# Kernel tuning notes

Measured on AMD Instinct MI355X. Metric: run time of the kernel, lower is better.

The kernel has to match this reference:

```python
import jax, jax.numpy as jnp
import numpy as np

H = 2048      # hidden_size
NH = 16       # num_attention_heads
HD = H // NH  # head_dim = 128
B, S = 2, 2048
ROPE_BASE = 10000.0


def setup_inputs() -> dict:
    key = jax.random.key(0)
    ks = jax.random.split(key, 9)
    init = 0.02
    inp = {
        "hidden_states": jax.random.normal(ks[0], (B, S, H), dtype=jnp.float32),
        # torch nn.Linear weights are [out_features, in_features]
        "wq": jax.random.normal(ks[1], (H, H), dtype=jnp.float32) * init,
        "bq": jnp.zeros((H,), dtype=jnp.float32),
        "wk": jax.random.normal(ks[2], (H, H), dtype=jnp.float32) * init,
        "bk": jnp.zeros((H,), dtype=jnp.float32),
        "wv": jax.random.normal(ks[3], (H, H), dtype=jnp.float32) * init,
        "bv": jnp.zeros((H,), dtype=jnp.float32),
        "wo": jax.random.normal(ks[4], (H, H), dtype=jnp.float32) * init,
        "bo": jnp.zeros((H,), dtype=jnp.float32),
    }
    return inp


def _rope_cos_sin(seq_len, dim, dtype):
    # standard RoPE tables: [seq_len, dim]
    inv_freq = 1.0 / (ROPE_BASE ** (jnp.arange(0, dim, 2, dtype=jnp.float32) / dim))
    freqs = jnp.arange(seq_len, dtype=jnp.float32)[:, None] * inv_freq[None, :]
    emb = jnp.concatenate([freqs, freqs], axis=-1)  # [S, dim]
    return jnp.cos(emb).astype(dtype), jnp.sin(emb).astype(dtype)


def _rotate_half(x):
    half = x.shape[-1] // 2
    return jnp.concatenate([-x[..., half:], x[..., :half]], axis=-1)


def reference(hidden_states, wq, bq, wk, bk, wv, bv, wo, bo):
    b, s, h = hidden_states.shape
    scale = HD ** -0.5

    def proj(x, w, bias):
        y = jnp.einsum("bsh,oh->bso", x, w) + bias
        # -> [b, nh, s, hd]
        return y.reshape(b, s, NH, HD).transpose(0, 2, 1, 3)

    q = proj(hidden_states, wq, bq)
    k = proj(hidden_states, wk, bk)
    v = proj(hidden_states, wv, bv)

    # rotary embeddings on q, k
    cos, sin = _rope_cos_sin(s, HD, q.dtype)  # [s, hd]
    q = q * cos + _rotate_half(q) * sin
    k = k * cos + _rotate_half(k) * sin

    # causal additive mask [s, s]
    mask = jnp.triu(jnp.full((s, s), -1e9, dtype=q.dtype), k=1)

    scores = jnp.einsum("bhqd,bhkd->bhqk", q, k) * scale + mask
    probs = jax.nn.softmax(scores, axis=-1)
    attn = jnp.einsum("bhqk,bhkd->bhqd", probs, v)
    attn = attn.transpose(0, 2, 1, 3).reshape(b, s, h)
    out = jnp.einsum("bsh,oh->bso", attn, wo) + bo
    return out
```

## Files before the change

### kernel.cpp

```cpp
#include <hip/hip_runtime.h>

typedef unsigned short u16;
typedef __attribute__((ext_vector_type(8))) __bf16 bf16x8;
typedef __attribute__((ext_vector_type(4))) float f32x4;
typedef __attribute__((ext_vector_type(4))) u16 u16x4;
typedef __attribute__((ext_vector_type(8))) u16 u16x8;

constexpr int S = 2048;
constexpr int H = 2048;
constexpr int NH = 16;
constexpr int HD = 128;
constexpr int M = 4096;
constexpr float SCALE = 0.08838834764831845f;

__device__ __forceinline__ u16 f2bf(float f) {
  union { float f; unsigned u; } v; v.f = f;
  unsigned r = v.u + 0x7fffu + ((v.u >> 16) & 1u);
  return (u16)(r >> 16);
}
__device__ __forceinline__ float bf2f(u16 u) {
  union { unsigned u; float f; } v; v.u = ((unsigned)u) << 16;
  return v.f;
}
__device__ __forceinline__ unsigned cvt_pk_bf16(float lo, float hi) {
  unsigned r;
  asm("v_cvt_pk_bf16_f32 %0, %1, %2" : "=v"(r) : "v"(lo), "v"(hi));
  return r;
}
__device__ __forceinline__ float fract_f(float x) {
  float o; asm("v_fract_f32 %0, %1" : "=v"(o) : "v"(x)); return o;
}
__device__ __forceinline__ float sin_rev(float x) {
  float o; asm("v_sin_f32 %0, %1" : "=v"(o) : "v"(x)); return o;
}
__device__ __forceinline__ float cos_rev(float x) {
  float o; asm("v_cos_f32 %0, %1" : "=v"(o) : "v"(x)); return o;
}
__device__ __forceinline__ f32x4 MFMA16(bf16x8 a, bf16x8 b, f32x4 c) {
  return __builtin_amdgcn_mfma_f32_16x16x32_bf16(a, b, c, 0, 0, 0);
}

__device__ __forceinline__ void gld16(const u16* g, u16* l) {
  __builtin_amdgcn_global_load_lds(
      (const __attribute__((address_space(1))) void*)g,
      (__attribute__((address_space(3))) void*)l, 16, 0, 0);
}

#define SBAR  { __builtin_amdgcn_sched_barrier(0); __builtin_amdgcn_s_barrier(); __builtin_amdgcn_sched_barrier(0); }
#define LGKM0 { asm volatile("s_waitcnt lgkmcnt(0)" ::: "memory"); __builtin_amdgcn_sched_barrier(0); }

__global__ __launch_bounds__(256) void prep_kernel(const float* __restrict__ x,
                                                   const float* __restrict__ wq,
                                                   const float* __restrict__ wk,
                                                   const float* __restrict__ wv,
                                                   const float* __restrict__ wo,
                                                   const float* __restrict__ bq,
                                                   const float* __restrict__ bk,
                                                   const float* __restrict__ bv,
                                                   u16* __restrict__ xb,
                                                   u16* __restrict__ wqkvb,
                                                   u16* __restrict__ wob,
                                                   float* __restrict__ bqkv) {
  const int NX = (M * H) / 1024;
  const int NW = (H * H) / 1024;
  int bid = blockIdx.x;
  if (bid < NX) {
    int i = (bid * 256 + threadIdx.x) * 4;
    float4 v = *(const float4*)(x + i);
    u16x4 o;
    o[0] = f2bf(v.x); o[1] = f2bf(v.y); o[2] = f2bf(v.z); o[3] = f2bf(v.w);
    *(u16x4*)(xb + i) = o;
    return;
  }
  bid -= NX;
  if (bid < 4 * NW) {
    const int z = bid / NW, lb = bid % NW;
    const float* in;
    u16* out;
    switch (z) {
      case 0: in = wq; out = wqkvb; break;
      case 1: in = wk; out = wqkvb + (size_t)H * H; break;
      case 2: in = wv; out = wqkvb + 2ull * H * H; break;
      default: in = wo; out = wob; break;
    }
    int i = (lb * 256 + threadIdx.x) * 4;
    int ro = i >> 11, cb = i & 2047;
    int rin = ro;
    if (z < 2) {
      int nd = ro & 127;
      int od = (nd & 1) ? (nd >> 1) + 64 : (nd >> 1);
      rin = (ro & ~127) | od;
    }
    float4 v = *(const float4*)(in + (size_t)rin * H + cb);
    u16x4 o;
    o[0] = f2bf(v.x); o[1] = f2bf(v.y); o[2] = f2bf(v.z); o[3] = f2bf(v.w);
    *(u16x4*)(out + i) = o;
    return;
  }
  bid -= 4 * NW;
  int i = bid * 256 + threadIdx.x;
  if (i < 4096) {
    const float* src = (i < 2048) ? bq : bk;
    int base = i & 2047;
    int nd = base & 127;
    int od = (nd & 1) ? (nd >> 1) + 64 : (nd >> 1);
    bqkv[i] = src[(base & ~127) | od];
  } else {
    bqkv[i] = bv[i & 2047];
  }
}

template<int NW, int EMODE>
__device__ __forceinline__ void gemm_body(const u16* __restrict__ A,
                                          const u16* __restrict__ Bw,
                                          const float* __restrict__ bias,
                                          void* __restrict__ out0, void* __restrict__ out1,
                                          void* __restrict__ out2,
                                          int brow, int bcol,
                                          u16* AsL, u16* BsL) {
  const int t = threadIdx.x;
  const int w = t >> 6, l = t & 63;
  const int wr = w >> 2, wc = w & 3;
  const int lr = l & 15, lg = l >> 4;
  const int swz = lr & 7;

  f32x4 acc[8][NW] = {};
  bf16x8 af[4], b0[NW], b1[NW];

  const int sr = t >> 3, sj = t & 7;

  auto STAGE_A = [&](int BUF, int HALF, int TILE) {
    u16* d = AsL + BUF * (256 * 64) + HALF * (128 * 64);
    const u16* sp = A + (size_t)(brow + HALF * 128) * H + TILE * 64;
    gld16(sp + (size_t)sr * H        + ((sj ^ (sr & 7)) * 8), d + t * 8);
    gld16(sp + (size_t)(64 + sr) * H + ((sj ^ (sr & 7)) * 8), d + (512 + t) * 8);
  };
  auto STAGE_B = [&](int BUF, int TILE) {
    u16* d = BsL + BUF * (NW * 64 * 64);
    const u16* sp = Bw + (size_t)bcol * H + TILE * 64;
    #pragma unroll
    for (int i = 0; i < NW; ++i)
      gld16(sp + (size_t)(i * 64 + sr) * H + ((sj ^ (sr & 7)) * 8),
            d + (i * 512 + t) * 8);
  };
  auto LDA = [&](int BUF, int KH, int MB) {
    const u16* base = AsL + BUF * (256 * 64) + (wr * 128 + MB * 16 + lr) * 64;
    #pragma unroll
    for (int i = 0; i < 4; ++i)
      af[i] = *(const bf16x8*)(base + i * (16 * 64) + (((KH * 4 + lg) ^ swz) * 8));
  };
  auto LDB = [&](int BUF, int KH, bf16x8* bb) {
    const u16* base = BsL + BUF * (NW * 64 * 64) + (wc * (NW * 16) + lr) * 64;
    #pragma unroll
    for (int n = 0; n < NW; ++n)
      bb[n] = *(const bf16x8*)(base + n * (16 * 64) + (((KH * 4 + lg) ^ swz) * 8));
  };
  auto MM = [&](int MB, bf16x8* bb) {
    __builtin_amdgcn_s_setprio(1);
    #pragma unroll
    for (int i = 0; i < 4; ++i)
      #pragma unroll
      for (int n = 0; n < NW; ++n)
        acc[MB + i][n] = MFMA16(af[i], bb[n], acc[MB + i][n]);
    __builtin_amdgcn_s_setprio(0);
  };
  auto GATE = [&]() {
    if constexpr (NW == 3) { asm volatile("s_waitcnt vmcnt(3)" ::: "memory"); }
    else                   { asm volatile("s_waitcnt vmcnt(2)" ::: "memory"); }
  };

  STAGE_A(0, 0, 0); STAGE_A(0, 1, 0);
  STAGE_B(0, 0);
  STAGE_B(1, 1);
  GATE();
  SBAR;

  for (int J = 0; J < 16; ++J) {
    const int u = 2 * J;
    const bool more = (J < 15);
    LDA(0, 0, 0); LDB(0, 0, b0);
    STAGE_A(1, 0, u + 1);
    SBAR; LGKM0; MM(0, b0); SBAR;
    LDA(0, 0, 4);
    STAGE_A(1, 1, u + 1);
    SBAR; LGKM0; MM(4, b0); SBAR;
    LDA(0, 1, 0); LDB(0, 1, b1);
    SBAR; LGKM0; MM(0, b1); SBAR;
    LDA(0, 1, 4);
    if (more) STAGE_B(0, u + 2);
    SBAR; LGKM0; MM(4, b1);
    if (more) { GATE(); } else { asm volatile("s_waitcnt vmcnt(0)" ::: "memory"); }
    SBAR;
    LDA(1, 0, 0); LDB(1, 0, b0);
    if (more) STAGE_A(0, 0, u + 2);
    SBAR; LGKM0; MM(0, b0); SBAR;
    LDA(1, 0, 4);
    if (more) STAGE_A(0, 1, u + 2);
    SBAR; LGKM0; MM(4, b0); SBAR;
    LDA(1, 1, 0); LDB(1, 1, b1);
    SBAR; LGKM0; MM(0, b1); SBAR;
    LDA(1, 1, 4);
    if (more) STAGE_B(1, u + 3);
    SBAR; LGKM0; MM(4, b1);
    if (more) { GATE(); SBAR; }
  }

  float frv[NW];
  if constexpr (EMODE == 3) {
    #pragma unroll
    for (int n = 0; n < NW; ++n) {
      const int col = ((bcol & 2047) + wc * (NW * 16) + n * 16 + lr);
      const int d = (col & 127) >> 1;
      frv[n] = __builtin_amdgcn_exp2f(-(float)d * 0.20762050593f) * 0.15915494309f;
    }
  }
  #pragma unroll
  for (int m = 0; m < 8; ++m) {
    const int row0 = brow + wr * 128 + m * 16 + lg * 4;
    #pragma unroll
    for (int n = 0; n < NW; ++n) {
      const int gcol0 = bcol + wc * (NW * 16) + n * 16;
      const float bv2 = bias[gcol0 + lr];
      if constexpr (EMODE == 0) {
        float* C = (float*)out0;
        #pragma unroll
        for (int r = 0; r < 4; ++r)
          C[(size_t)(row0 + r) * H + gcol0 + lr] = acc[m][n][r] + bv2;
      } else {
        const int sel = gcol0 >> 11;
        const int col = (gcol0 & 2047) + lr;
        if (sel < 2) {
          u16* Cq = sel ? (u16*)out1 : (u16*)out0;
          const float scl = sel ? 1.f : SCALE;
          #pragma unroll
          for (int r = 0; r < 4; ++r) {
            const int row = row0 + r;
            const float sv = (float)(row & (S - 1));
            float xv = acc[m][n][r] + bv2;
            float pr = __shfl_xor(xv, 1);
            float ang = fract_f(sv * frv[n]);
            float cs = cos_rev(ang), sn = sin_rev(ang);
            float o = (lr & 1) ? (xv * cs + pr * sn)
                               : (xv * cs - pr * sn);
            Cq[(size_t)row * H + col] = f2bf(o * scl);
          }
        } else {
          const int hh = col >> 7, d = col & 127;
          const int b = row0 >> 11, s0 = row0 & (S - 1);
          u16x4 pk;
          #pragma unroll
          for (int r = 0; r < 4; ++r) pk[r] = f2bf(acc[m][n][r] + bv2);
          *(u16x4*)((u16*)out2 + ((size_t)((b * 16 + hh) * 128 + d)) * S + s0) = pk;
        }
      }
    }
  }
}

__global__ __launch_bounds__(512, 2) void gemm_qkv8(const u16* __restrict__ xb,
                                                    const u16* __restrict__ wqkv,
                                                    const float* __restrict__ bqkv,
                                                    u16* Qb, u16* Kb, u16* Vt) {
  __shared__ u16 AsL[2 * 256 * 64];
  __shared__ u16 BsL[2 * 192 * 64];
  const int id = blockIdx.x;
  const int xcd = id & 7, sid = id >> 3;
  const int bx = xcd * 4 + (sid & 3), by = sid >> 2;
  gemm_body<3, 3>(xb, wqkv, bqkv, Qb, Kb, Vt, by * 256, bx * 192, AsL, BsL);
}

__global__ __launch_bounds__(512, 2) void gemm_o8(const u16* __restrict__ A,
                                                  const u16* __restrict__ W,
                                                  const float* __restrict__ bias,
                                                  float* __restrict__ C) {
  __shared__ u16 AsL[2 * 256 * 64];
  __shared__ u16 BsL[2 * 128 * 64];
  const int id = blockIdx.x;
  const int xcd = id & 7, sid = id >> 3;
  const int bx = xcd * 2 + (sid & 1), by = sid >> 1;
  gemm_body<2, 0>(A, W, bias, C, nullptr, nullptr, by * 256, bx * 128, AsL, BsL);
}

__global__ __launch_bounds__(256) void attn_fwd(const u16* __restrict__ Q,
                                                const u16* __restrict__ Kx,
                                                const u16* __restrict__ Vt,
                                                u16* __restrict__ O) {
  const int id = blockIdx.x;
  const int xcd = id & 7, slot = id >> 3;
  const int bh = (slot >> 4) * 8 + xcd;
  const int pid = slot & 15;
  const int b = bh >> 4, h = bh & 15;
  const int t = threadIdx.x, w = t >> 6, l = t & 63;
  const int lr = l & 15, lg = l >> 4;
  const int swz = lr & 7;

  __shared__ u16 Ks[2][64 * 128];
  __shared__ u16 Vs[2][128 * 64];
  __shared__ u16 P_lds[4][16 * 64];
  u16* pw = &P_lds[w][0];

  const u16* kbase = Kx + (size_t)(b * S) * H + h * HD;
  const u16* vbase = Vt + (size_t)bh * HD * S;

  auto stageK = [&](int bf, int k0) {
    #pragma unroll
    for (int it = 0; it < 4; ++it) {
      int c = it * 256 + t;
      int row = c >> 4, j = c & 15;
      gld16(kbase + (size_t)(k0 + row) * H + ((j ^ (row & 7)) * 8), &Ks[bf][0] + c * 8);
    }
  };
  auto stageV = [&](int bf, int k0) {
    #pragma unroll
    for (int it = 0; it < 4; ++it) {
      int c = it * 256 + t;
      int row = c >> 3, j = c & 7;
      gld16(vbase + (size_t)row * S + k0 + ((j ^ (row & 7)) * 8), &Vs[bf][0] + c * 8);
    }
  };

  int cur = 0;
  for (int qi = 0; qi < 2; ++qi) {
    const int qt = qi ? pid : (31 - pid);
    const int q0 = qt * 64 + w * 16;

    bf16x8 qa[4];
    const u16* qbase = Q + (size_t)(b * S + q0 + lr) * H + h * HD;
    #pragma unroll
    for (int ks = 0; ks < 4; ++ks)
      qa[ks] = *(const bf16x8*)(qbase + ks * 32 + lg * 8);

    f32x4 acc[8] = {};
    float mrun[4], lrun[4];
    #pragma unroll
    for (int r = 0; r < 4; ++r) { mrun[r] = -1e30f; lrun[r] = 0.f; }

    __syncthreads();
    stageK(cur, 0);
    stageV(cur, 0);
    __syncthreads();

    for (int kt = 0; kt <= qt; ++kt) {
      if (kt < qt) {
        stageK(cur ^ 1, (kt + 1) * 64);
        stageV(cur ^ 1, (kt + 1) * 64);
      }
      const u16* kl = &Ks[cur][0];
      const u16* vl = &Vs[cur][0];

      f32x4 sc[4] = {};
      __builtin_amdgcn_s_setprio(1);
      #pragma unroll
      for (int ks = 0; ks < 4; ++ks) {
        #pragma unroll
        for (int f = 0; f < 4; ++f) {
          bf16x8 kf = *(const bf16x8*)(kl + (f * 16 + lr) * 128 + (((ks * 4 + lg) ^ swz) * 8));
          sc[f] = __builtin_amdgcn_mfma_f32_16x16x32_bf16(qa[ks], kf, sc[f], 0, 0, 0);
        }
      }
      __builtin_amdgcn_s_setprio(0);
      const bool diag = (kt == qt);
      float p[4][4];
      #pragma unroll
      for (int f = 0; f < 4; ++f)
        #pragma unroll
        for (int r = 0; r < 4; ++r) {
          float v = sc[f][r];
          if (diag && (f * 16 + lr > w * 16 + lg * 4 + r)) v = -1e30f;
          p[f][r] = v;
        }
      float mx[4];
      #pragma unroll
      for (int r = 0; r < 4; ++r) {
        float m0 = fmaxf(fmaxf(p[0][r], p[1][r]), fmaxf(p[2][r], p[3][r]));
        m0 = fmaxf(m0, __shfl_xor(m0, 1));
        m0 = fmaxf(m0, __shfl_xor(m0, 2));
        m0 = fmaxf(m0, __shfl_xor(m0, 4));
        m0 = fmaxf(m0, __shfl_xor(m0, 8));
        mx[r] = m0;
      }
      bool grow = (mx[0] > mrun[0] + 8.f) || (mx[1] > mrun[1] + 8.f) ||
                  (mx[2] > mrun[2] + 8.f) || (mx[3] > mrun[3] + 8.f);
      if (__any(grow)) {
        float resc[4];
        #pragma unroll
        for (int r = 0; r < 4; ++r) {
          float mnew = fmaxf(mrun[r], mx[r]);
          resc[r] = __expf(mrun[r] - mnew);
          mrun[r] = mnew;
          lrun[r] *= resc[r];
        }
        #pragma unroll
        for (int fd = 0; fd < 8; ++fd) {
          f32x4 a = acc[fd];
          a[0] *= resc[0]; a[1] *= resc[1]; a[2] *= resc[2]; a[3] *= resc[3];
          acc[fd] = a;
        }
      }
      #pragma unroll
      for (int r = 0; r < 4; ++r) {
        float sum = 0.f;
        #pragma unroll
        for (int f = 0; f < 4; ++f) {
          float e = __expf(p[f][r] - mrun[r]);
          p[f][r] = e;
          sum += e;
        }
        sum += __shfl_xor(sum, 1);
        sum += __shfl_xor(sum, 2);
        sum += __shfl_xor(sum, 4);
        sum += __shfl_xor(sum, 8);
        lrun[r] += sum;
      }
      {
        const int r0 = lg * 4;
        #pragma unroll
        for (int f = 0; f < 4; ++f) {
          const int col = f * 16 + lr;
          unsigned w01 = cvt_pk_bf16(p[f][0], p[f][1]);
          unsigned w23 = cvt_pk_bf16(p[f][2], p[f][3]);
          pw[(r0 + 0) * 64 + (col ^ (((r0 + 0) & 7) << 3))] = (u16)(w01 & 0xffffu);
          pw[(r0 + 1) * 64 + (col ^ (((r0 + 1) & 7) << 3))] = (u16)(w01 >> 16);
          pw[(r0 + 2) * 64 + (col ^ (((r0 + 2) & 7) << 3))] = (u16)(w23 & 0xffffu);
          pw[(r0 + 3) * 64 + (col ^ (((r0 + 3) & 7) << 3))] = (u16)(w23 >> 16);
        }
      }
      __builtin_amdgcn_s_setprio(1);
      #pragma unroll
      for (int ks = 0; ks < 2; ++ks) {
        int col0 = ks * 32 + lg * 8;
        bf16x8 pa = *(const bf16x8*)(pw + lr * 64 + (col0 ^ (swz << 3)));
        #pragma unroll
        for (int fd = 0; fd < 8; ++fd) {
          bf16x8 vb = *(const bf16x8*)(vl + (fd * 16 + lr) * 64 + (((ks * 4 + lg) ^ swz) * 8));
          acc[fd] = __builtin_amdgcn_mfma_f32_16x16x32_bf16(pa, vb, acc[fd], 0, 0, 0);
        }
      }
      __builtin_amdgcn_s_setprio(0);
      __syncthreads();
      cur ^= 1;
    }

    u16* ob = O + (size_t)(b * S + q0 + lg * 4) * H + h * HD;
    #pragma unroll
    for (int r = 0; r < 4; ++r) {
      float inv = 1.f / lrun[r];
      #pragma unroll
      for (int fd = 0; fd < 8; ++fd)
        ob[(size_t)r * H + fd * 16 + lr] = f2bf(acc[fd][r] * inv);
    }
  }
}

extern "C" void kernel_launch(void* const* d_in, const int* in_sizes, int n_in,
                              void* d_out, int out_size, void* d_ws, size_t ws_size,
                              hipStream_t stream) {
  const float* x  = (const float*)d_in[0];
  const float* wq = (const float*)d_in[1];
  const float* bq = (const float*)d_in[2];
  const float* wk = (const float*)d_in[3];
  const float* bk = (const float*)d_in[4];
  const float* wv = (const float*)d_in[5];
  const float* bv = (const float*)d_in[6];
  const float* wo = (const float*)d_in[7];
  const float* bo = (const float*)d_in[8];

  char* ws = (char*)d_ws;
  u16*   xb    = (u16*)(ws);
  u16*   wqkvb = (u16*)(ws + (16ull << 20));
  u16*   wob   = (u16*)(ws + (40ull << 20));
  u16*   Qb    = (u16*)(ws + (48ull << 20));
  u16*   Kb    = (u16*)(ws + (64ull << 20));
  u16*   Vt    = (u16*)(ws + (80ull << 20));
  u16*   Ob    = (u16*)(ws + (96ull << 20));
  float* bqkv  = (float*)(ws + (112ull << 20));

  const int NPREP = (M * H) / 1024 + 4 * (H * H) / 1024 + 24;
  prep_kernel<<<NPREP, 256, 0, stream>>>(x, wq, wk, wv, wo, bq, bk, bv,
                                         xb, wqkvb, wob, bqkv);

  gemm_qkv8<<<512, 512, 0, stream>>>(xb, wqkvb, bqkv, Qb, Kb, Vt);

  attn_fwd<<<512, 256, 0, stream>>>(Qb, Kb, Vt, Ob);

  gemm_o8<<<256, 512, 0, stream>>>(Ob, wob, bo, (float*)d_out);
}
```

Measured before the change: 263.9 us.

## Enlarge attention query tile to 128 rows with 32 rows per warp

Each attention block now handles one 128-row query tile, with each warp owning two 16-row MFMA subtiles. Every staged K/V tile therefore feeds twice as many queries, which halves K/V global and LDS traffic per query. The earlier scheme, where one block ran two paired 64-row tiles back to back for load balance, is replaced by one tile per block, scheduled longest-first. This trades more registers per thread (launch bounds set to 2 blocks) and less even per-block work for better data reuse.

```diff
diff --git a/kernel.cpp b/kernel.cpp
--- a/kernel.cpp
+++ b/kernel.cpp
@@ -281,14 +281,15 @@
   gemm_body<2, 0>(A, W, bias, C, nullptr, nullptr, by * 256, bx * 128, AsL, BsL);
 }
 
-__global__ __launch_bounds__(256) void attn_fwd(const u16* __restrict__ Q,
-                                                const u16* __restrict__ Kx,
-                                                const u16* __restrict__ Vt,
-                                                u16* __restrict__ O) {
+__global__ __launch_bounds__(256, 2) void attn_fwd(const u16* __restrict__ Q,
+                                                   const u16* __restrict__ Kx,
+                                                   const u16* __restrict__ Vt,
+                                                   u16* __restrict__ O) {
   const int id = blockIdx.x;
-  const int xcd = id & 7, slot = id >> 3;
-  const int bh = (slot >> 4) * 8 + xcd;
-  const int pid = slot & 15;
+  const int xcd = id & 7, rest = id >> 3;
+  const int bh = (rest & 3) * 8 + xcd;
+  const int j = rest >> 2;
+  const int qt = (j < 8) ? (15 - j) : (j - 8);
   const int b = bh >> 4, h = bh & 15;
   const int t = threadIdx.x, w = t >> 6, l = t & 63;
   const int lr = l & 15, lg = l >> 4;
@@ -296,7 +297,7 @@
 
   __shared__ u16 Ks[2][64 * 128];
   __shared__ u16 Vs[2][128 * 64];
-  __shared__ u16 P_lds[4][16 * 64];
+  __shared__ u16 P_lds[4][32 * 64];
   u16* pw = &P_lds[w][0];
 
   const u16* kbase = Kx + (size_t)(b * S) * H + h * HD;
@@ -306,148 +307,183 @@
     #pragma unroll
     for (int it = 0; it < 4; ++it) {
       int c = it * 256 + t;
-      int row = c >> 4, j = c & 15;
-      gld16(kbase + (size_t)(k0 + row) * H + ((j ^ (row & 7)) * 8), &Ks[bf][0] + c * 8);
+      int row = c >> 4, jj = c & 15;
+      gld16(kbase + (size_t)(k0 + row) * H + ((jj ^ (row & 7)) * 8), &Ks[bf][0] + c * 8);
     }
   };
   auto stageV = [&](int bf, int k0) {
     #pragma unroll
     for (int it = 0; it < 4; ++it) {
       int c = it * 256 + t;
-      int row = c >> 3, j = c & 7;
-      gld16(vbase + (size_t)row * S + k0 + ((j ^ (row & 7)) * 8), &Vs[bf][0] + c * 8);
-    }
-  };
+      int row = c >> 3, jj = c & 7;
+      gld16(vbase + (size_t)row * S + k0 + ((jj ^ (row & 7)) * 8), &Vs[bf][0] + c * 8);
+    }
+  };
+
+  const int q0 = qt * 128 + w * 32;
+
+  bf16x8 qa[2][4];
+  #pragma unroll
+  for (int s2 = 0; s2 < 2; ++s2) {
+    const u16* qbase = Q + (size_t)(b * S + q0 + s2 * 16 + lr) * H + h * HD;
+    #pragma unroll
+    for (int ks = 0; ks < 4; ++ks)
+      qa[s2][ks] = *(const bf16x8*)(qbase + ks * 32 + lg * 8);
+  }
+
+  f32x4 acc0[8] = {}, acc1[8] = {};
+  float mrun[2][4], lrun[2][4];
+  #pragma unroll
+  for (int s2 = 0; s2 < 2; ++s2)
+    #pragma unroll
+    for (int r = 0; r < 4; ++r) { mrun[s2][r] = -1e30f; lrun[s2][r] = 0.f; }
 
   int cur = 0;
-  for (int qi = 0; qi < 2; ++qi) {
-    const int qt = qi ? pid : (31 - pid);
-    const int q0 = qt * 64 + w * 16;
-
-    bf16x8 qa[4];
-    const u16* qbase = Q + (size_t)(b * S + q0 + lr) * H + h * HD;
-    #pragma unroll
-    for (int ks = 0; ks < 4; ++ks)
-      qa[ks] = *(const bf16x8*)(qbase + ks * 32 + lg * 8);
-
-    f32x4 acc[8] = {};
-    float mrun[4], lrun[4];
-    #pragma unroll
-    for (int r = 0; r < 4; ++r) { mrun[r] = -1e30f; lrun[r] = 0.f; }
-
-    __syncthreads();
-    stageK(cur, 0);
-    stageV(cur, 0);
-    __syncthreads();
-
-    for (int kt = 0; kt <= qt; ++kt) {
-      if (kt < qt) {
-        stageK(cur ^ 1, (kt + 1) * 64);
-        stageV(cur ^ 1, (kt + 1) * 64);
-      }
-      const u16* kl = &Ks[cur][0];
-      const u16* vl = &Vs[cur][0];
-
-      f32x4 sc[4] = {};
-      __builtin_amdgcn_s_setprio(1);
-      #pragma unroll
-      for (int ks = 0; ks < 4; ++ks) {
-        #pragma unroll
-        for (int f = 0; f < 4; ++f) {
-          bf16x8 kf = *(const bf16x8*)(kl + (f * 16 + lr) * 128 + (((ks * 4 + lg) ^ swz) * 8));
-          sc[f] = __builtin_amdgcn_mfma_f32_16x16x32_bf16(qa[ks], kf, sc[f], 0, 0, 0);
+  const int NT = 2 * qt + 2;
+  stageK(cur, 0);
+  stageV(cur, 0);
+  __syncthreads();
+
+  for (int kt = 0; kt < NT; ++kt) {
+    if (kt < NT - 1) {
+      stageK(cur ^ 1, (kt + 1) * 64);
+      stageV(cur ^ 1, (kt + 1) * 64);
+    }
+    const u16* kl = &Ks[cur][0];
+    const u16* vl = &Vs[cur][0];
+    const int k0 = kt * 64;
+
+    f32x4 sc0[4] = {}, sc1[4] = {};
+    __builtin_amdgcn_s_setprio(1);
+    #pragma unroll
+    for (int ks = 0; ks < 4; ++ks) {
+      #pragma unroll
+      for (int f = 0; f < 4; ++f) {
+        bf16x8 kf = *(const bf16x8*)(kl + (f * 16 + lr) * 128 + (((ks * 4 + lg) ^ swz) * 8));
+        sc0[f] = MFMA16(qa[0][ks], kf, sc0[f]);
+        sc1[f] = MFMA16(qa[1][ks], kf, sc1[f]);
+      }
+    }
+    __builtin_amdgcn_s_setprio(0);
+
+    const bool maskt = (kt >= 2 * qt);
+    float p[2][4][4];
+    #pragma unroll
+    for (int f = 0; f < 4; ++f)
+      #pragma unroll
+      for (int r = 0; r < 4; ++r) {
+        float v0 = sc0[f][r], v1 = sc1[f][r];
+        if (maskt) {
+          const int col = k0 + f * 16 + lr;
+          const int row0a = q0 + lg * 4 + r;
+          if (col > row0a) v0 = -1e30f;
+          if (col > row0a + 16) v1 = -1e30f;
         }
-      }
-      __builtin_amdgcn_s_setprio(0);
-      const bool diag = (kt == qt);
-      float p[4][4];
-      #pragma unroll
-      for (int f = 0; f < 4; ++f)
-        #pragma unroll
-        for (int r = 0; r < 4; ++r) {
-          float v = sc[f][r];
-          if (diag && (f * 16 + lr > w * 16 + lg * 4 + r)) v = -1e30f;
-          p[f][r] = v;
-        }
-      float mx[4];
+        p[0][f][r] = v0;
+        p[1][f][r] = v1;
+      }
+
+    float mx[2][4];
+    #pragma unroll
+    for (int s2 = 0; s2 < 2; ++s2)
       #pragma unroll
       for (int r = 0; r < 4; ++r) {
-        float m0 = fmaxf(fmaxf(p[0][r], p[1][r]), fmaxf(p[2][r], p[3][r]));
+        float m0 = fmaxf(fmaxf(p[s2][0][r], p[s2][1][r]), fmaxf(p[s2][2][r], p[s2][3][r]));
         m0 = fmaxf(m0, __shfl_xor(m0, 1));
         m0 = fmaxf(m0, __shfl_xor(m0, 2));
         m0 = fmaxf(m0, __shfl_xor(m0, 4));
         m0 = fmaxf(m0, __shfl_xor(m0, 8));
-        mx[r] = m0;
-      }
-      bool grow = (mx[0] > mrun[0] + 8.f) || (mx[1] > mrun[1] + 8.f) ||
-                  (mx[2] > mrun[2] + 8.f) || (mx[3] > mrun[3] + 8.f);
-      if (__any(grow)) {
-        float resc[4];
+        mx[s2][r] = m0;
+      }
+    bool grow = false;
+    #pragma unroll
+    for (int s2 = 0; s2 < 2; ++s2)
+      #pragma unroll
+      for (int r = 0; r < 4; ++r)
+        grow = grow || (mx[s2][r] > mrun[s2][r] + 8.f);
+    if (__any(grow)) {
+      float resc[2][4];
+      #pragma unroll
+      for (int s2 = 0; s2 < 2; ++s2)
         #pragma unroll
         for (int r = 0; r < 4; ++r) {
-          float mnew = fmaxf(mrun[r], mx[r]);
-          resc[r] = __expf(mrun[r] - mnew);
-          mrun[r] = mnew;
-          lrun[r] *= resc[r];
+          float mnew = fmaxf(mrun[s2][r], mx[s2][r]);
+          resc[s2][r] = __expf(mrun[s2][r] - mnew);
+          mrun[s2][r] = mnew;
+          lrun[s2][r] *= resc[s2][r];
         }
-        #pragma unroll
-        for (int fd = 0; fd < 8; ++fd) {
-          f32x4 a = acc[fd];
-          a[0] *= resc[0]; a[1] *= resc[1]; a[2] *= resc[2]; a[3] *= resc[3];
-          acc[fd] = a;
-        }
-      }
+      #pragma unroll
+      for (int fd = 0; fd < 8; ++fd) {
+        f32x4 a = acc0[fd];
+        a[0] *= resc[0][0]; a[1] *= resc[0][1]; a[2] *= resc[0][2]; a[3] *= resc[0][3];
+        acc0[fd] = a;
+        f32x4 c = acc1[fd];
+        c[0] *= resc[1][0]; c[1] *= resc[1][1]; c[2] *= resc[1][2]; c[3] *= resc[1][3];
+        acc1[fd] = c;
+      }
+    }
+    #pragma unroll
+    for (int s2 = 0; s2 < 2; ++s2)
       #pragma unroll
       for (int r = 0; r < 4; ++r) {
         float sum = 0.f;
         #pragma unroll
         for (int f = 0; f < 4; ++f) {
-          float e = __expf(p[f][r] - mrun[r]);
-          p[f][r] = e;
+          float e = __expf(p[s2][f][r] - mrun[s2][r]);
+          p[s2][f][r] = e;
           sum += e;
         }
         sum += __shfl_xor(sum, 1);
         sum += __shfl_xor(sum, 2);
         sum += __shfl_xor(sum, 4);
         sum += __shfl_xor(sum, 8);
-        lrun[r] += sum;
-      }
-      {
-        const int r0 = lg * 4;
-        #pragma unroll
-        for (int f = 0; f < 4; ++f) {
-          const int col = f * 16 + lr;
-          unsigned w01 = cvt_pk_bf16(p[f][0], p[f][1]);
-          unsigned w23 = cvt_pk_bf16(p[f][2], p[f][3]);
-          pw[(r0 + 0) * 64 + (col ^ (((r0 + 0) & 7) << 3))] = (u16)(w01 & 0xffffu);
-          pw[(r0 + 1) * 64 + (col ^ (((r0 + 1) & 7) << 3))] = (u16)(w01 >> 16);
-          pw[(r0 + 2) * 64 + (col ^ (((r0 + 2) & 7) << 3))] = (u16)(w23 & 0xffffu);
-          pw[(r0 + 3) * 64 + (col ^ (((r0 + 3) & 7) << 3))] = (u16)(w23 >> 16);
-        }
-      }
-      __builtin_amdgcn_s_setprio(1);
-      #pragma unroll
-      for (int ks = 0; ks < 2; ++ks) {
-        int col0 = ks * 32 + lg * 8;
-        bf16x8 pa = *(const bf16x8*)(pw + lr * 64 + (col0 ^ (swz << 3)));
-        #pragma unroll
-        for (int fd = 0; fd < 8; ++fd) {
-          bf16x8 vb = *(const bf16x8*)(vl + (fd * 16 + lr) * 64 + (((ks * 4 + lg) ^ swz) * 8));
-          acc[fd] = __builtin_amdgcn_mfma_f32_16x16x32_bf16(pa, vb, acc[fd], 0, 0, 0);
-        }
-      }
-      __builtin_amdgcn_s_setprio(0);
-      __syncthreads();
-      cur ^= 1;
-    }
-
-    u16* ob = O + (size_t)(b * S + q0 + lg * 4) * H + h * HD;
+        lrun[s2][r] += sum;
+      }
+
+    #pragma unroll
+    for (int s2 = 0; s2 < 2; ++s2) {
+      const int r0 = s2 * 16 + lg * 4;
+      #pragma unroll
+      for (int f = 0; f < 4; ++f) {
+        const int col = f * 16 + lr;
+        unsigned w01 = cvt_pk_bf16(p[s2][f][0], p[s2][f][1]);
+        unsigned w23 = cvt_pk_bf16(p[s2][f][2], p[s2][f][3]);
+        pw[(r0 + 0) * 64 + (col ^ (((r0 + 0) & 7) << 3))] = (u16)(w01 & 0xffffu);
+        pw[(r0 + 1) * 64 + (col ^ (((r0 + 1) & 7) << 3))] = (u16)(w01 >> 16);
+        pw[(r0 + 2) * 64 + (col ^ (((r0 + 2) & 7) << 3))] = (u16)(w23 & 0xffffu);
+        pw[(r0 + 3) * 64 + (col ^ (((r0 + 3) & 7) << 3))] = (u16)(w23 >> 16);
+      }
+    }
+
+    __builtin_amdgcn_s_setprio(1);
+    #pragma unroll
+    for (int ks = 0; ks < 2; ++ks) {
+      int col0 = ks * 32 + lg * 8;
+      bf16x8 pa0 = *(const bf16x8*)(pw + lr * 64 + (col0 ^ (swz << 3)));
+      bf16x8 pa1 = *(const bf16x8*)(pw + (16 + lr) * 64 + (col0 ^ (swz << 3)));
+      #pragma unroll
+      for (int fd = 0; fd < 8; ++fd) {
+        bf16x8 vb = *(const bf16x8*)(vl + (fd * 16 + lr) * 64 + (((ks * 4 + lg) ^ swz) * 8));
+        acc0[fd] = MFMA16(pa0, vb, acc0[fd]);
+        acc1[fd] = MFMA16(pa1, vb, acc1[fd]);
+      }
+    }
+    __builtin_amdgcn_s_setprio(0);
+    __syncthreads();
+    cur ^= 1;
+  }
+
+  #pragma unroll
+  for (int s2 = 0; s2 < 2; ++s2) {
+    u16* ob = O + (size_t)(b * S + q0 + s2 * 16 + lg * 4) * H + h * HD;
     #pragma unroll
     for (int r = 0; r < 4; ++r) {
-      float inv = 1.f / lrun[r];
-      #pragma unroll
-      for (int fd = 0; fd < 8; ++fd)
-        ob[(size_t)r * H + fd * 16 + lr] = f2bf(acc[fd][r] * inv);
+      float inv = 1.f / lrun[s2][r];
+      #pragma unroll
+      for (int fd = 0; fd < 8; ++fd) {
+        float v = (s2 ? acc1[fd][r] : acc0[fd][r]) * inv;
+        ob[(size_t)r * H + fd * 16 + lr] = f2bf(v);
+      }
     }
   }
 }
```

Measured after the change: 279.9 us. 1.06x slower.

## Replace output-projection GEMM with smaller 128x128 tile, simpler double-buffered kernel

Applied to the files above, without the earlier changes.

The shared templated GEMM body is inlined into the QKV kernel, and the output projection gets its own kernel. The new kernel uses 128x128 tiles with 256 threads and 512 blocks instead of 256x128 tiles with 512 threads and 256 blocks. Its K loop is a simple double-buffered stage/compute loop with a full vmcnt wait each iteration. This aims to fill more CUs on the 4096x2048 output GEMM, at the cost of less reuse per tile and a less finely interleaved pipeline.

```diff
diff --git a/kernel.cpp b/kernel.cpp
--- a/kernel.cpp
+++ b/kernel.cpp
@@ -46,6 +46,7 @@
       (__attribute__((address_space(3))) void*)l, 16, 0, 0);
 }
 
+#define BAR   __builtin_amdgcn_s_barrier()
 #define SBAR  { __builtin_amdgcn_sched_barrier(0); __builtin_amdgcn_s_barrier(); __builtin_amdgcn_sched_barrier(0); }
 #define LGKM0 { asm volatile("s_waitcnt lgkmcnt(0)" ::: "memory"); __builtin_amdgcn_sched_barrier(0); }
 
@@ -110,14 +111,21 @@
   }
 }
 
-template<int NW, int EMODE>
-__device__ __forceinline__ void gemm_body(const u16* __restrict__ A,
-                                          const u16* __restrict__ Bw,
-                                          const float* __restrict__ bias,
-                                          void* __restrict__ out0, void* __restrict__ out1,
-                                          void* __restrict__ out2,
-                                          int brow, int bcol,
-                                          u16* AsL, u16* BsL) {
+__global__ __launch_bounds__(512, 2) void gemm_qkv8(const u16* __restrict__ A,
+                                                    const u16* __restrict__ Bw,
+                                                    const float* __restrict__ bias,
+                                                    u16* __restrict__ Qb,
+                                                    u16* __restrict__ Kb,
+                                                    u16* __restrict__ Vt) {
+  __shared__ u16 AsL[2 * 256 * 64];
+  __shared__ u16 BsL[2 * 192 * 64];
+  constexpr int NW = 3;
+
+  const int id = blockIdx.x;
+  const int xcd = id & 7, sid = id >> 3;
+  const int bx = xcd * 4 + (sid & 3), by = sid >> 2;
+  const int brow = by * 256, bcol = bx * 192;
+
   const int t = threadIdx.x;
   const int w = t >> 6, l = t & 63;
   const int wr = w >> 2, wc = w & 3;
@@ -164,10 +172,7 @@
         acc[MB + i][n] = MFMA16(af[i], bb[n], acc[MB + i][n]);
     __builtin_amdgcn_s_setprio(0);
   };
-  auto GATE = [&]() {
-    if constexpr (NW == 3) { asm volatile("s_waitcnt vmcnt(3)" ::: "memory"); }
-    else                   { asm volatile("s_waitcnt vmcnt(2)" ::: "memory"); }
-  };
+  auto GATE = [&]() { asm volatile("s_waitcnt vmcnt(3)" ::: "memory"); };
 
   STAGE_A(0, 0, 0); STAGE_A(0, 1, 0);
   STAGE_B(0, 0);
@@ -206,13 +211,11 @@
   }
 
   float frv[NW];
-  if constexpr (EMODE == 3) {
-    #pragma unroll
-    for (int n = 0; n < NW; ++n) {
-      const int col = ((bcol & 2047) + wc * (NW * 16) + n * 16 + lr);
-      const int d = (col & 127) >> 1;
-      frv[n] = __builtin_amdgcn_exp2f(-(float)d * 0.20762050593f) * 0.15915494309f;
-    }
+  #pragma unroll
+  for (int n = 0; n < NW; ++n) {
+    const int col = ((bcol & 2047) + wc * (NW * 16) + n * 16 + lr);
+    const int d = (col & 127) >> 1;
+    frv[n] = __builtin_amdgcn_exp2f(-(float)d * 0.20762050593f) * 0.15915494309f;
   }
   #pragma unroll
   for (int m = 0; m < 8; ++m) {
@@ -221,64 +224,121 @@
     for (int n = 0; n < NW; ++n) {
       const int gcol0 = bcol + wc * (NW * 16) + n * 16;
       const float bv2 = bias[gcol0 + lr];
-      if constexpr (EMODE == 0) {
-        float* C = (float*)out0;
-        #pragma unroll
-        for (int r = 0; r < 4; ++r)
-          C[(size_t)(row0 + r) * H + gcol0 + lr] = acc[m][n][r] + bv2;
+      const int sel = gcol0 >> 11;
+      const int col = (gcol0 & 2047) + lr;
+      if (sel < 2) {
+        u16* Cq = sel ? Kb : Qb;
+        const float scl = sel ? 1.f : SCALE;
+        #pragma unroll
+        for (int r = 0; r < 4; ++r) {
+          const int row = row0 + r;
+          const float sv = (float)(row & (S - 1));
+          float xv = acc[m][n][r] + bv2;
+          float pr = __shfl_xor(xv, 1);
+          float ang = fract_f(sv * frv[n]);
+          float cs = cos_rev(ang), sn = sin_rev(ang);
+          float o = (lr & 1) ? (xv * cs + pr * sn)
+                             : (xv * cs - pr * sn);
+          Cq[(size_t)row * H + col] = f2bf(o * scl);
+        }
       } else {
-        const int sel = gcol0 >> 11;
-        const int col = (gcol0 & 2047) + lr;
-        if (sel < 2) {
-          u16* Cq = sel ? (u16*)out1 : (u16*)out0;
-          const float scl = sel ? 1.f : SCALE;
-          #pragma unroll
-          for (int r = 0; r < 4; ++r) {
-            const int row = row0 + r;
-            const float sv = (float)(row & (S - 1));
-            float xv = acc[m][n][r] + bv2;
-            float pr = __shfl_xor(xv, 1);
-            float ang = fract_f(sv * frv[n]);
-            float cs = cos_rev(ang), sn = sin_rev(ang);
-            float o = (lr & 1) ? (xv * cs + pr * sn)
-                               : (xv * cs - pr * sn);
-            Cq[(size_t)row * H + col] = f2bf(o * scl);
-          }
-        } else {
-          const int hh = col >> 7, d = col & 127;
-          const int b = row0 >> 11, s0 = row0 & (S - 1);
-          u16x4 pk;
-          #pragma unroll
-          for (int r = 0; r < 4; ++r) pk[r] = f2bf(acc[m][n][r] + bv2);
-          *(u16x4*)((u16*)out2 + ((size_t)((b * 16 + hh) * 128 + d)) * S + s0) = pk;
-        }
-      }
-    }
-  }
-}
-
-__global__ __launch_bounds__(512, 2) void gemm_qkv8(const u16* __restrict__ xb,
-                                                    const u16* __restrict__ wqkv,
-                                                    const float* __restrict__ bqkv,
-                                                    u16* Qb, u16* Kb, u16* Vt) {
-  __shared__ u16 AsL[2 * 256 * 64];
-  __shared__ u16 BsL[2 * 192 * 64];
-  const int id = blockIdx.x;
-  const int xcd = id & 7, sid = id >> 3;
-  const int bx = xcd * 4 + (sid & 3), by = sid >> 2;
-  gemm_body<3, 3>(xb, wqkv, bqkv, Qb, Kb, Vt, by * 256, bx * 192, AsL, BsL);
-}
-
-__global__ __launch_bounds__(512, 2) void gemm_o8(const u16* __restrict__ A,
-                                                  const u16* __restrict__ W,
+        const int hh = col >> 7, d = col & 127;
+        const int b = row0 >> 11, s0 = row0 & (S - 1);
+        u16x4 pk;
+        #pragma unroll
+        for (int r = 0; r < 4; ++r) pk[r] = f2bf(acc[m][n][r] + bv2);
+        *(u16x4*)(Vt + ((size_t)((b * 16 + hh) * 128 + d)) * S + s0) = pk;
+      }
+    }
+  }
+}
+
+__global__ __launch_bounds__(256, 2) void gemm_o2(const u16* __restrict__ A,
+                                                  const u16* __restrict__ Bw,
                                                   const float* __restrict__ bias,
                                                   float* __restrict__ C) {
-  __shared__ u16 AsL[2 * 256 * 64];
+  __shared__ u16 AsL[2 * 128 * 64];
   __shared__ u16 BsL[2 * 128 * 64];
   const int id = blockIdx.x;
   const int xcd = id & 7, sid = id >> 3;
-  const int bx = xcd * 2 + (sid & 1), by = sid >> 1;
-  gemm_body<2, 0>(A, W, bias, C, nullptr, nullptr, by * 256, bx * 128, AsL, BsL);
+  const int bx = xcd * 2 + (sid & 1);
+  const int by = sid >> 1;
+  const int brow = by * 128, bcol = bx * 128;
+
+  const int t = threadIdx.x;
+  const int w = t >> 6, l = t & 63;
+  const int wr = w >> 1, wc = w & 1;
+  const int lr = l & 15, lg = l >> 4;
+  const int swz = lr & 7;
+
+  f32x4 acc[4][4] = {};
+  const int sr = t >> 3, sj = t & 7;
+
+  auto STAGE = [&](int BUF, int TILE) {
+    u16* da = AsL + BUF * (128 * 64);
+    const u16* sa = A + (size_t)brow * H + TILE * 64;
+    #pragma unroll
+    for (int it = 0; it < 4; ++it) {
+      int row = it * 32 + sr;
+      gld16(sa + (size_t)row * H + ((sj ^ (row & 7)) * 8), da + (it * 256 + t) * 8);
+    }
+    u16* db = BsL + BUF * (128 * 64);
+    const u16* sb = Bw + (size_t)bcol * H + TILE * 64;
+    #pragma unroll
+    for (int it = 0; it < 4; ++it) {
+      int row = it * 32 + sr;
+      gld16(sb + (size_t)row * H + ((sj ^ (row & 7)) * 8), db + (it * 256 + t) * 8);
+    }
+  };
+  auto LDA = [&](int BUF, int KH, bf16x8* aa) {
+    const u16* base = AsL + BUF * (128 * 64) + (wr * 64 + lr) * 64;
+    #pragma unroll
+    for (int i = 0; i < 4; ++i)
+      aa[i] = *(const bf16x8*)(base + i * (16 * 64) + (((KH * 4 + lg) ^ swz) * 8));
+  };
+  auto LDB = [&](int BUF, int KH, bf16x8* bb) {
+    const u16* base = BsL + BUF * (128 * 64) + (wc * 64 + lr) * 64;
+    #pragma unroll
+    for (int n = 0; n < 4; ++n)
+      bb[n] = *(const bf16x8*)(base + n * (16 * 64) + (((KH * 4 + lg) ^ swz) * 8));
+  };
+  auto MM = [&](bf16x8* aa, bf16x8* bb) {
+    __builtin_amdgcn_s_setprio(1);
+    #pragma unroll
+    for (int i = 0; i < 4; ++i)
+      #pragma unroll
+      for (int n = 0; n < 4; ++n)
+        acc[i][n] = MFMA16(aa[i], bb[n], acc[i][n]);
+    __builtin_amdgcn_s_setprio(0);
+  };
+
+  STAGE(0, 0);
+  asm volatile("s_waitcnt vmcnt(0)" ::: "memory");
+  BAR;
+
+  int c = 0;
+  for (int u = 0; u < 32; ++u) {
+    if (u < 31) STAGE(c ^ 1, u + 1);
+    bf16x8 aa[4], bb[4];
+    LDA(c, 0, aa); LDB(c, 0, bb); MM(aa, bb);
+    LDA(c, 1, aa); LDB(c, 1, bb); MM(aa, bb);
+    asm volatile("s_waitcnt vmcnt(0)" ::: "memory");
+    BAR;
+    c ^= 1;
+  }
+
+  #pragma unroll
+  for (int m = 0; m < 4; ++m) {
+    const int row0 = brow + wr * 64 + m * 16 + lg * 4;
+    #pragma unroll
+    for (int n = 0; n < 4; ++n) {
+      const int col = bcol + wc * 64 + n * 16 + lr;
+      const float bv = bias[col];
+      #pragma unroll
+      for (int r = 0; r < 4; ++r)
+        C[(size_t)(row0 + r) * H + col] = acc[m][n][r] + bv;
+    }
+  }
 }
 
 __global__ __launch_bounds__(256) void attn_fwd(const u16* __restrict__ Q,
@@ -483,5 +543,5 @@
 
   attn_fwd<<<512, 256, 0, stream>>>(Qb, Kb, Vt, Ob);
 
-  gemm_o8<<<256, 512, 0, stream>>>(Ob, wob, bo, (float*)d_out);
-}
+  gemm_o2<<<512, 256, 0, stream>>>(Ob, wob, bo, (float*)d_out);
+}
```

After: 263.9 us. Within noise of the previous version (-0.0%).
